# Kernel tuning notes

Hardware: AMD Instinct MI355X
Metric: run time of the kernel (lower is better)

The kernel has to match this reference:

```python
import jax, jax.numpy as jnp
import numpy as np

N = 50000        # nodes
E = 1600000      # edges (avg degree 32)
H = 128          # hidden_channels == num_filters
G = 50           # num_gaussians
L = 5            # num_interactions
CUTOFF = 4.5
VOCAB = 100
LOG2 = float(np.log(2.0))


def setup_inputs() -> dict:
    key = jax.random.key(0)
    ks = jax.random.split(key, 12)
    s = 1.0 / np.sqrt(H)
    sg = 1.0 / np.sqrt(G)
    atomic_numbers = jax.random.randint(ks[0], (N,), 0, VOCAB, dtype=jnp.int32)
    edge_index = jax.random.randint(ks[1], (2, E), 0, N, dtype=jnp.int32)
    edge_attr = jax.random.uniform(ks[2], (E,), dtype=jnp.float32)
    emb = jax.random.normal(ks[3], (VOCAB, H), dtype=jnp.float32) * 0.1
    emb = emb.at[0].set(0.0)  # padding_idx=0
    Wi = jax.random.normal(ks[4], (L, H, H), dtype=jnp.float32) * s
    bi = jnp.zeros((L, H), dtype=jnp.float32)
    Wn = jax.random.normal(ks[5], (L, G, H), dtype=jnp.float32) * sg
    bn = jnp.zeros((L, H), dtype=jnp.float32)
    Wo = jax.random.normal(ks[6], (L, H, H), dtype=jnp.float32) * s
    bo = jnp.zeros((L, H), dtype=jnp.float32)
    Wl = jax.random.normal(ks[7], (L, H, H), dtype=jnp.float32) * s
    bl = jnp.zeros((L, H), dtype=jnp.float32)
    return {"atomic_numbers": atomic_numbers, "edge_index": edge_index,
            "edge_attr": edge_attr, "emb": emb,
            "Wi": Wi, "bi": bi, "Wn": Wn, "bn": bn,
            "Wo": Wo, "bo": bo, "Wl": Wl, "bl": bl}


def _gaussian_smearing(dist):
    offsets = jnp.linspace(0.0, CUTOFF, G, dtype=jnp.float32)
    coeff = -0.5 / (offsets[1] - offsets[0]) ** 2
    return jnp.exp(coeff * (dist[:, None] - offsets[None, :]) ** 2)  # [E, G]


def reference(atomic_numbers, edge_index, edge_attr, emb,
              Wi, bi, Wn, bn, Wo, bo, Wl, bl):
    src, dst = edge_index[0], edge_index[1]
    x = emb[atomic_numbers]                      # [N, H]
    gauss = _gaussian_smearing(edge_attr)        # [E, G]
    C = 0.5 * (jnp.cos(edge_attr * jnp.pi / CUTOFF) + 1.0)  # cosine cutoff [E]
    for l in range(L):
        W = (gauss @ Wn[l] + bn[l]) * C[:, None]   # edge filters [E, H]
        h = x @ Wi[l] + bi[l]                       # [N, H]
        msg = h[src] * W                            # gather + filter [E, H]
        agg = jax.ops.segment_sum(msg, dst, num_segments=N)  # scatter-add [N, H]
        h = agg @ Wo[l] + bo[l]
        h = jax.nn.softplus(h) - LOG2               # shifted softplus
        h = h @ Wl[l] + bl[l]
        x = x + h                                   # residual
    return x
```

## Files before the change

kernel.cpp:

```cpp
#include <hip/hip_runtime.h>
#include <hip/hip_bf16.h>

#define HDIM 128
#define NG 50
#define NL 5
#define TBN 4096
#define CAP 96
#define CAPB 9000
#define CHUNK 8192

static constexpr float CUTOFF_F = 4.5f;
static constexpr float PI_F = 3.14159265358979323846f;
static constexpr float LN2_F = 0.6931471805599453f;

typedef __attribute__((ext_vector_type(8))) short bf16x8;
typedef __attribute__((ext_vector_type(4))) float f32x4;

__device__ __forceinline__ unsigned f2bfbits(float f) {
    unsigned b = __float_as_uint(f);
    return (b + 0x7FFFu + ((b >> 16) & 1u)) >> 16;
}
__device__ __forceinline__ float bflo(unsigned u) { return __uint_as_float(u << 16); }
__device__ __forceinline__ float bfhi(unsigned u) { return __uint_as_float(u & 0xFFFF0000u); }

__device__ __forceinline__ float softplus_shifted(float v) {
    return fmaxf(v, 0.0f) + __logf(1.0f + __expf(-fabsf(v))) - LN2_F;
}

__device__ __forceinline__ bf16x8 ldB(const unsigned short* __restrict__ W,
                                      int nn, int kc, int l4) {
    return *reinterpret_cast<const bf16x8*>(W + nn * HDIM + kc * 32 + l4 * 8);
}

__global__ __launch_bounds__(256) void embed_kernel(
    const int* __restrict__ an, const float* __restrict__ emb,
    float* __restrict__ x, int n)
{
    int idx = blockIdx.x * 256 + threadIdx.x;
    int total = n * (HDIM / 4);
    if (idx >= total) return;
    int i = idx >> 5;
    int j = idx & 31;
    int a = an[i];
    reinterpret_cast<float4*>(x)[(size_t)i * 32 + j] =
        reinterpret_cast<const float4*>(emb)[(size_t)a * 32 + j];
}

__global__ __launch_bounds__(256) void prep_weights(
    const float* __restrict__ Wi, const float* __restrict__ Wo,
    const float* __restrict__ Wl, unsigned short* __restrict__ Wt)
{
    int b = blockIdx.x;
    int l = b / 3, m = b % 3;
    const float* src = (m == 0 ? Wi : (m == 1 ? Wo : Wl)) + (size_t)l * HDIM * HDIM;
    unsigned short* dst = Wt + (size_t)b * HDIM * HDIM;
    for (int idx = threadIdx.x; idx < HDIM * HDIM; idx += 256) {
        int k = idx >> 7, n = idx & 127;
        dst[n * HDIM + k] = (unsigned short)f2bfbits(src[k * HDIM + n]);
    }
}

__global__ __launch_bounds__(128) void build_tables_all(
    const float* __restrict__ Wn, const float* __restrict__ bn,
    unsigned short* __restrict__ T)
{
    __shared__ float gs[NG];
    int p = blockIdx.x;
    int l = blockIdx.y;
    int j = threadIdx.x;
    const float* Wnl = Wn + (size_t)l * NG * HDIM;
    float d = (float)p * (1.0f / (float)TBN);
    if (j < NG) {
        const float delta = CUTOFF_F / (float)(NG - 1);
        const float coeff = -0.5f / (delta * delta);
        float t = d - (float)j * delta;
        gs[j] = expf(coeff * t * t);
    }
    __syncthreads();
    float acc = bn[(size_t)l * HDIM + j];
    #pragma unroll 10
    for (int g = 0; g < NG; ++g) acc = fmaf(gs[g], Wnl[g * HDIM + j], acc);
    acc *= 0.5f * (cosf(d * (PI_F / CUTOFF_F)) + 1.0f);
    T[((size_t)l * (TBN + 1) + p) * HDIM + j] = (unsigned short)f2bfbits(acc);
}

__global__ __launch_bounds__(512) void bucket_pass(
    const int* __restrict__ src, const int* __restrict__ dstp,
    const float* __restrict__ attr, int* __restrict__ gbase,
    uint2* __restrict__ buf, int E, int nbuck)
{
    __shared__ int hist[256], cur[256], base_l[256];
    const int tid = threadIdx.x;
    if (tid < 256) { hist[tid] = 0; cur[tid] = 0; }
    __syncthreads();
    const int e0 = blockIdx.x * CHUNK;
    const int e1 = min(e0 + CHUNK, E);
    for (int e = e0 + tid; e < e1; e += 512)
        atomicAdd(&hist[dstp[e] >> 8], 1);
    __syncthreads();
    if (tid < nbuck)
        base_l[tid] = hist[tid] ? atomicAdd(&gbase[tid], hist[tid]) : 0;
    __syncthreads();
    for (int e = e0 + tid; e < e1; e += 512) {
        int d = dstp[e];
        int b = d >> 8;
        int rank = atomicAdd(&cur[b], 1);
        int pos = base_l[b] + rank;
        unsigned ii = (unsigned)(int)fminf(attr[e] * (float)TBN + 0.5f, (float)TBN);
        if (pos < CAPB)
            buf[(size_t)b * CAPB + pos] = make_uint2((ii << 16) | (unsigned)src[e], (unsigned)d);
    }
}

__global__ __launch_bounds__(512) void bin_pass(
    const int* __restrict__ gtot, const uint2* __restrict__ buf,
    unsigned* __restrict__ sp, int* __restrict__ cnt, int N)
{
    __shared__ int cl[256];
    const int b = blockIdx.x;
    const int tid = threadIdx.x;
    if (tid < 256) cl[tid] = 0;
    __syncthreads();
    int total = gtot[b];
    if (total > CAPB) total = CAPB;
    const uint2* rb = buf + (size_t)b * CAPB;
    for (int i = tid; i < total; i += 512) {
        uint2 r = rb[i];
        int node = (int)r.y;
        int slot = atomicAdd(&cl[node & 255], 1);
        if (slot < CAP) sp[(size_t)node * CAP + slot] = r.x;
    }
    __syncthreads();
    if (tid < 256) {
        int node = b * 256 + tid;
        if (node < N) cnt[node] = min(cl[tid], CAP);
    }
}

__global__ __launch_bounds__(256) void mfma_gemm0(
    const float* __restrict__ A, const unsigned short* __restrict__ Wt,
    const float* __restrict__ bias, unsigned short* __restrict__ outp, int M)
{
    __shared__ unsigned short Ls[64 * HDIM];
    const int tid = threadIdx.x;
    const int row0 = blockIdx.x * 64;

    #pragma unroll
    for (int it = 0; it < 8; ++it) {
        int idx = it * 256 + tid;
        int r = idx >> 5;
        int k2 = (idx & 31) * 8;
        int row = row0 + r;
        float4 v = make_float4(0.f, 0.f, 0.f, 0.f);
        if (row < M) v = reinterpret_cast<const float4*>(A)[(size_t)row * 32 + (idx & 31)];
        uint2 u;
        u.x = f2bfbits(v.x) | (f2bfbits(v.y) << 16);
        u.y = f2bfbits(v.z) | (f2bfbits(v.w) << 16);
        *reinterpret_cast<uint2*>(reinterpret_cast<char*>(Ls) +
            r * 256 + (k2 ^ ((r & 7) << 4))) = u;
    }
    __syncthreads();

    const int wid = tid >> 6, lane = tid & 63;
    const int wr = wid >> 1, wc = wid & 1;
    const int l15 = lane & 15, l4 = lane >> 4;

    f32x4 acc[2][4] = {};
    bf16x8 afrag[2][4];
    #pragma unroll
    for (int m = 0; m < 2; ++m)
        #pragma unroll
        for (int kc = 0; kc < 4; ++kc) {
            int r = wr * 32 + m * 16 + l15;
            int k2 = (kc * 32 + l4 * 8) * 2;
            afrag[m][kc] = *reinterpret_cast<const bf16x8*>(
                reinterpret_cast<const char*>(Ls) + r * 256 + (k2 ^ ((r & 7) << 4)));
        }
    __syncthreads();
    #pragma unroll
    for (int n = 0; n < 4; ++n)
        #pragma unroll
        for (int kc = 0; kc < 4; ++kc) {
            bf16x8 bfrag = ldB(Wt, wc * 64 + n * 16 + l15, kc, l4);
            #pragma unroll
            for (int m = 0; m < 2; ++m)
                acc[m][n] = __builtin_amdgcn_mfma_f32_16x16x32_bf16(
                    afrag[m][kc], bfrag, acc[m][n], 0, 0, 0);
        }
    #pragma unroll
    for (int n = 0; n < 4; ++n) {
        int col = wc * 64 + n * 16 + l15;
        float bv = bias[col];
        #pragma unroll
        for (int m = 0; m < 2; ++m)
            #pragma unroll
            for (int r = 0; r < 4; ++r) {
                int rl = wr * 32 + m * 16 + l4 * 4 + r;
                Ls[rl * HDIM + col] = (unsigned short)f2bfbits(acc[m][n][r] + bv);
            }
    }
    __syncthreads();
    #pragma unroll
    for (int it = 0; it < 4; ++it) {
        int e = it * 256 + tid;
        int row = row0 + (e >> 4);
        if (row < M)
            reinterpret_cast<uint4*>(outp)[(size_t)row0 * 16 + e] =
                reinterpret_cast<const uint4*>(Ls)[e];
    }
}

template<int LAST>
__global__ __launch_bounds__(512) void gemm_fused(
    const unsigned short* __restrict__ aggb, const unsigned short* __restrict__ Wot,
    const float* __restrict__ bo, const unsigned short* __restrict__ Wlt,
    const float* __restrict__ bl, float* __restrict__ x,
    const unsigned short* __restrict__ Wit, const float* __restrict__ bi_,
    unsigned short* __restrict__ hb, int M)
{
    __shared__ unsigned short Ls[64 * HDIM];
    const int tid = threadIdx.x;
    const int row0 = blockIdx.x * 64;
    const int wid = tid >> 6, lane = tid & 63;
    const int wr = wid >> 1, wc = wid & 1;
    const int l15 = lane & 15, l4 = lane >> 4;

    const unsigned short* ag =
        aggb + (size_t)(row0 + wr * 16 + l15) * HDIM + l4 * 8;
    f32x4 acc1[4] = {};
    bf16x8 af[4];
    #pragma unroll
    for (int kc = 0; kc < 4; ++kc)
        af[kc] = *reinterpret_cast<const bf16x8*>(ag + kc * 32);
    #pragma unroll
    for (int n = 0; n < 4; ++n)
        #pragma unroll
        for (int kc = 0; kc < 4; ++kc) {
            bf16x8 bfrag = ldB(Wot, wc * 64 + n * 16 + l15, kc, l4);
            acc1[n] = __builtin_amdgcn_mfma_f32_16x16x32_bf16(af[kc], bfrag, acc1[n], 0, 0, 0);
        }

    #pragma unroll
    for (int n = 0; n < 4; ++n) {
        int col = wc * 64 + n * 16 + l15;
        float bv = bo[col];
        #pragma unroll
        for (int r = 0; r < 4; ++r) {
            int rl = wr * 16 + l4 * 4 + r;
            float v = softplus_shifted(acc1[n][r] + bv);
            *reinterpret_cast<unsigned short*>(reinterpret_cast<char*>(Ls) +
                rl * 256 + ((2 * col) ^ ((rl & 7) << 4))) = (unsigned short)f2bfbits(v);
        }
    }
    __syncthreads();

    {
        int r = wr * 16 + l15;
        #pragma unroll
        for (int kc = 0; kc < 4; ++kc) {
            int k2 = (kc * 32 + l4 * 8) * 2;
            af[kc] = *reinterpret_cast<const bf16x8*>(
                reinterpret_cast<const char*>(Ls) + r * 256 + (k2 ^ ((r & 7) << 4)));
        }
    }
    __syncthreads();
    f32x4 acc2[4] = {};
    #pragma unroll
    for (int n = 0; n < 4; ++n)
        #pragma unroll
        for (int kc = 0; kc < 4; ++kc) {
            bf16x8 bfrag = ldB(Wlt, wc * 64 + n * 16 + l15, kc, l4);
            acc2[n] = __builtin_amdgcn_mfma_f32_16x16x32_bf16(af[kc], bfrag, acc2[n], 0, 0, 0);
        }

    #pragma unroll
    for (int n = 0; n < 4; ++n) {
        int col = wc * 64 + n * 16 + l15;
        float bv = bl[col];
        #pragma unroll
        for (int r = 0; r < 4; ++r) {
            int rl = wr * 16 + l4 * 4 + r;
            int row = row0 + rl;
            float v = acc2[n][r] + bv;
            if (row < M) {
                float* o = x + (size_t)row * HDIM + col;
                v += *o;
                *o = v;
            }
            if (!LAST)
                *reinterpret_cast<unsigned short*>(reinterpret_cast<char*>(Ls) +
                    rl * 256 + ((2 * col) ^ ((rl & 7) << 4))) = (unsigned short)f2bfbits(v);
        }
    }
    if (LAST) return;
    __syncthreads();

    {
        int r = wr * 16 + l15;
        #pragma unroll
        for (int kc = 0; kc < 4; ++kc) {
            int k2 = (kc * 32 + l4 * 8) * 2;
            af[kc] = *reinterpret_cast<const bf16x8*>(
                reinterpret_cast<const char*>(Ls) + r * 256 + (k2 ^ ((r & 7) << 4)));
        }
    }
    __syncthreads();
    f32x4 acc3[4] = {};
    #pragma unroll
    for (int n = 0; n < 4; ++n)
        #pragma unroll
        for (int kc = 0; kc < 4; ++kc) {
            bf16x8 bfrag = ldB(Wit, wc * 64 + n * 16 + l15, kc, l4);
            acc3[n] = __builtin_amdgcn_mfma_f32_16x16x32_bf16(af[kc], bfrag, acc3[n], 0, 0, 0);
        }
    #pragma unroll
    for (int n = 0; n < 4; ++n) {
        int col = wc * 64 + n * 16 + l15;
        float bv = bi_[col];
        #pragma unroll
        for (int r = 0; r < 4; ++r) {
            int rl = wr * 16 + l4 * 4 + r;
            Ls[rl * HDIM + col] = (unsigned short)f2bfbits(acc3[n][r] + bv);
        }
    }
    __syncthreads();
    #pragma unroll
    for (int it = 0; it < 2; ++it) {
        int e = it * 512 + tid;
        int row = row0 + (e >> 4);
        if (row < M)
            reinterpret_cast<uint4*>(hb)[(size_t)row0 * 16 + e] =
                reinterpret_cast<const uint4*>(Ls)[e];
    }
}

__global__ __launch_bounds__(256) void agg_kernel(
    const int* __restrict__ cnt, const unsigned* __restrict__ sp,
    const unsigned short* __restrict__ T,
    const unsigned* __restrict__ hb,
    unsigned* __restrict__ aggb, int n)
{
    __shared__ float2 part[2][64];
    const int tid = threadIdx.x;
    const int lane = tid & 63;
    const int wv = tid >> 6;
    const int pair = wv >> 1, half = wv & 1;
    const int node = blockIdx.x * 2 + pair;

    int deg = (node < n) ? cnt[node] : 0;
    const unsigned* recs = sp + (size_t)node * CAP;
    int d2 = deg >> 1;
    int i  = half ? d2 : 0;
    int i1 = half ? deg : d2;
    float ax = 0.0f, ay = 0.0f;

    for (; i + 8 <= i1; i += 8) {
        unsigned rec[8], tv[8], hv[8];
        #pragma unroll
        for (int k = 0; k < 8; ++k) rec[k] = recs[i + k];
        #pragma unroll
        for (int k = 0; k < 8; ++k) {
            tv[k] = reinterpret_cast<const unsigned*>(T + (size_t)(rec[k] >> 16) * HDIM)[lane];
            hv[k] = hb[(size_t)(rec[k] & 0xFFFFu) * 64 + lane];
        }
        #pragma unroll
        for (int k = 0; k < 8; ++k) {
            ax = fmaf(bflo(hv[k]), bflo(tv[k]), ax);
            ay = fmaf(bfhi(hv[k]), bfhi(tv[k]), ay);
        }
    }
    if (i + 4 <= i1) {
        unsigned rec[4], tv[4], hv[4];
        #pragma unroll
        for (int k = 0; k < 4; ++k) rec[k] = recs[i + k];
        #pragma unroll
        for (int k = 0; k < 4; ++k) {
            tv[k] = reinterpret_cast<const unsigned*>(T + (size_t)(rec[k] >> 16) * HDIM)[lane];
            hv[k] = hb[(size_t)(rec[k] & 0xFFFFu) * 64 + lane];
        }
        #pragma unroll
        for (int k = 0; k < 4; ++k) {
            ax = fmaf(bflo(hv[k]), bflo(tv[k]), ax);
            ay = fmaf(bfhi(hv[k]), bfhi(tv[k]), ay);
        }
        i += 4;
    }
    for (; i < i1; ++i) {
        unsigned rec = recs[i];
        unsigned tvv = reinterpret_cast<const unsigned*>(T + (size_t)(rec >> 16) * HDIM)[lane];
        unsigned hvv = hb[(size_t)(rec & 0xFFFFu) * 64 + lane];
        ax = fmaf(bflo(hvv), bflo(tvv), ax);
        ay = fmaf(bfhi(hvv), bfhi(tvv), ay);
    }

    if (half) part[pair][lane] = make_float2(ax, ay);
    __syncthreads();
    if (!half && node < n) {
        float2 p = part[pair][lane];
        ax += p.x; ay += p.y;
        aggb[(size_t)node * 64 + lane] = f2bfbits(ax) | (f2bfbits(ay) << 16);
    }
}

extern "C" void kernel_launch(void* const* d_in, const int* in_sizes, int n_in,
                              void* d_out, int out_size, void* d_ws, size_t ws_size,
                              hipStream_t stream)
{
    const int*   an   = (const int*)d_in[0];
    const int*   ei   = (const int*)d_in[1];
    const float* attr = (const float*)d_in[2];
    const float* emb  = (const float*)d_in[3];
    const float* Wi   = (const float*)d_in[4];
    const float* bi   = (const float*)d_in[5];
    const float* Wn   = (const float*)d_in[6];
    const float* bn   = (const float*)d_in[7];
    const float* Wo   = (const float*)d_in[8];
    const float* bo   = (const float*)d_in[9];
    const float* Wl   = (const float*)d_in[10];
    const float* bl   = (const float*)d_in[11];

    const int N = in_sizes[0];
    const int E = in_sizes[2];
    const int* srcp = ei;
    const int* dstp = ei + E;
    const int nbuck = (N + 255) >> 8;

    float* x = (float*)d_out;

    char* w = (char*)d_ws;
    unsigned*       aggb = (unsigned*)w;      w += (size_t)N * HDIM * 2;
    unsigned*       hb   = (unsigned*)w;      w += (size_t)N * HDIM * 2;
    unsigned short* T    = (unsigned short*)w; w += (size_t)NL * (TBN + 1) * HDIM * 2;
    unsigned short* Wt   = (unsigned short*)w; w += (size_t)NL * 3 * HDIM * HDIM * 2;
    int*            cnt  = (int*)w;           w += (size_t)N * 4;
    int*            gbase= (int*)w;           w += 256 * 4;
    unsigned*       sp   = (unsigned*)w;      w += (size_t)N * CAP * 4;
    uint2*          buf  = (uint2*)aggb;

    prep_weights<<<NL * 3, 256, 0, stream>>>(Wi, Wo, Wl, Wt);
    embed_kernel<<<(N * 32 + 255) / 256, 256, 0, stream>>>(an, emb, x, N);
    build_tables_all<<<dim3(TBN + 1, NL), 128, 0, stream>>>(Wn, bn, T);

    hipMemsetAsync(gbase, 0, 256 * sizeof(int), stream);
    bucket_pass<<<(E + CHUNK - 1) / CHUNK, 512, 0, stream>>>(
        srcp, dstp, attr, gbase, buf, E, nbuck);
    bin_pass<<<nbuck, 512, 0, stream>>>(gbase, buf, sp, cnt, N);

    const int gemm_grid = (N + 63) / 64;
    const int agg_grid  = (N + 1) / 2;

    mfma_gemm0<<<gemm_grid, 256, 0, stream>>>(x, Wt, bi, (unsigned short*)hb, N);

    for (int l = 0; l < NL; ++l) {
        agg_kernel<<<agg_grid, 256, 0, stream>>>(
            cnt, sp, T + (size_t)l * (TBN + 1) * HDIM, hb, aggb, N);
        if (l < NL - 1) {
            gemm_fused<0><<<gemm_grid, 512, 0, stream>>>(
                (unsigned short*)aggb, Wt + (size_t)(l * 3 + 1) * HDIM * HDIM, bo + (size_t)l * HDIM,
                Wt + (size_t)(l * 3 + 2) * HDIM * HDIM, bl + (size_t)l * HDIM, x,
                Wt + (size_t)((l + 1) * 3 + 0) * HDIM * HDIM, bi + (size_t)(l + 1) * HDIM,
                (unsigned short*)hb, N);
        } else {
            gemm_fused<1><<<gemm_grid, 512, 0, stream>>>(
                (unsigned short*)aggb, Wt + (size_t)(l * 3 + 1) * HDIM * HDIM, bo + (size_t)l * HDIM,
                Wt + (size_t)(l * 3 + 2) * HDIM * HDIM, bl + (size_t)l * HDIM, x,
                Wt, bi, (unsigned short*)hb, N);
        }
    }
}
```

Baseline: 835.5 us.

## Restructure aggregation to one wave per node with 16-byte gathers

Measured after the change: 757.7 us. 9.3% less time.

```diff
diff --git a/kernel.cpp b/kernel.cpp
--- a/kernel.cpp
+++ b/kernel.cpp
@@ -94,15 +94,22 @@
     if (tid < 256) { hist[tid] = 0; cur[tid] = 0; }
     __syncthreads();
     const int e0 = blockIdx.x * CHUNK;
-    const int e1 = min(e0 + CHUNK, E);
-    for (int e = e0 + tid; e < e1; e += 512)
-        atomicAdd(&hist[dstp[e] >> 8], 1);
+    int myd[CHUNK / 512];
+    #pragma unroll
+    for (int k = 0; k < CHUNK / 512; ++k) {
+        int e = e0 + k * 512 + tid;
+        myd[k] = (e < E) ? dstp[e] : -1;
+        if (myd[k] >= 0) atomicAdd(&hist[myd[k] >> 8], 1);
+    }
     __syncthreads();
     if (tid < nbuck)
         base_l[tid] = hist[tid] ? atomicAdd(&gbase[tid], hist[tid]) : 0;
     __syncthreads();
-    for (int e = e0 + tid; e < e1; e += 512) {
-        int d = dstp[e];
+    #pragma unroll
+    for (int k = 0; k < CHUNK / 512; ++k) {
+        int d = myd[k];
+        if (d < 0) continue;
+        int e = e0 + k * 512 + tid;
         int b = d >> 8;
         int rank = atomicAdd(&cur[b], 1);
         int pos = base_l[b] + rank;
@@ -334,71 +341,69 @@
     }
 }
 
+#define ACC8(hv, tv) \
+    a0 = fmaf(bflo(hv.x), bflo(tv.x), a0); a1 = fmaf(bfhi(hv.x), bfhi(tv.x), a1); \
+    a2 = fmaf(bflo(hv.y), bflo(tv.y), a2); a3 = fmaf(bfhi(hv.y), bfhi(tv.y), a3); \
+    a4 = fmaf(bflo(hv.z), bflo(tv.z), a4); a5 = fmaf(bfhi(hv.z), bfhi(tv.z), a5); \
+    a6 = fmaf(bflo(hv.w), bflo(tv.w), a6); a7 = fmaf(bfhi(hv.w), bfhi(tv.w), a7);
+
 __global__ __launch_bounds__(256) void agg_kernel(
     const int* __restrict__ cnt, const unsigned* __restrict__ sp,
     const unsigned short* __restrict__ T,
     const unsigned* __restrict__ hb,
     unsigned* __restrict__ aggb, int n)
 {
-    __shared__ float2 part[2][64];
     const int tid = threadIdx.x;
     const int lane = tid & 63;
-    const int wv = tid >> 6;
-    const int pair = wv >> 1, half = wv & 1;
-    const int node = blockIdx.x * 2 + pair;
-
-    int deg = (node < n) ? cnt[node] : 0;
+    const int g = lane >> 4;
+    const int c16 = lane & 15;
+    const int node = (blockIdx.x * 256 + tid) >> 6;
+    if (node >= n) return;
+
+    const int deg = cnt[node];
     const unsigned* recs = sp + (size_t)node * CAP;
-    int d2 = deg >> 1;
-    int i  = half ? d2 : 0;
-    int i1 = half ? deg : d2;
-    float ax = 0.0f, ay = 0.0f;
-
-    for (; i + 8 <= i1; i += 8) {
-        unsigned rec[8], tv[8], hv[8];
-        #pragma unroll
-        for (int k = 0; k < 8; ++k) rec[k] = recs[i + k];
-        #pragma unroll
-        for (int k = 0; k < 8; ++k) {
-            tv[k] = reinterpret_cast<const unsigned*>(T + (size_t)(rec[k] >> 16) * HDIM)[lane];
-            hv[k] = hb[(size_t)(rec[k] & 0xFFFFu) * 64 + lane];
-        }
-        #pragma unroll
-        for (int k = 0; k < 8; ++k) {
-            ax = fmaf(bflo(hv[k]), bflo(tv[k]), ax);
-            ay = fmaf(bfhi(hv[k]), bfhi(tv[k]), ay);
-        }
-    }
-    if (i + 4 <= i1) {
-        unsigned rec[4], tv[4], hv[4];
-        #pragma unroll
-        for (int k = 0; k < 4; ++k) rec[k] = recs[i + k];
-        #pragma unroll
-        for (int k = 0; k < 4; ++k) {
-            tv[k] = reinterpret_cast<const unsigned*>(T + (size_t)(rec[k] >> 16) * HDIM)[lane];
-            hv[k] = hb[(size_t)(rec[k] & 0xFFFFu) * 64 + lane];
-        }
-        #pragma unroll
-        for (int k = 0; k < 4; ++k) {
-            ax = fmaf(bflo(hv[k]), bflo(tv[k]), ax);
-            ay = fmaf(bfhi(hv[k]), bfhi(tv[k]), ay);
-        }
-        i += 4;
-    }
-    for (; i < i1; ++i) {
-        unsigned rec = recs[i];
-        unsigned tvv = reinterpret_cast<const unsigned*>(T + (size_t)(rec >> 16) * HDIM)[lane];
-        unsigned hvv = hb[(size_t)(rec & 0xFFFFu) * 64 + lane];
-        ax = fmaf(bflo(hvv), bflo(tvv), ax);
-        ay = fmaf(bfhi(hvv), bfhi(tvv), ay);
-    }
-
-    if (half) part[pair][lane] = make_float2(ax, ay);
-    __syncthreads();
-    if (!half && node < n) {
-        float2 p = part[pair][lane];
-        ax += p.x; ay += p.y;
-        aggb[(size_t)node * 64 + lane] = f2bfbits(ax) | (f2bfbits(ay) << 16);
+    const uint4* T4 = reinterpret_cast<const uint4*>(T);
+    const uint4* h4 = reinterpret_cast<const uint4*>(hb);
+
+    float a0 = 0.f, a1 = 0.f, a2 = 0.f, a3 = 0.f;
+    float a4 = 0.f, a5 = 0.f, a6 = 0.f, a7 = 0.f;
+
+    int i = 0;
+    for (; i + 8 <= deg; i += 8) {
+        unsigned ra = recs[i + g];
+        unsigned rb = recs[i + 4 + g];
+        uint4 ta = T4[(size_t)(ra >> 16) * 16 + c16];
+        uint4 ha = h4[(size_t)(ra & 0xFFFFu) * 16 + c16];
+        uint4 tb = T4[(size_t)(rb >> 16) * 16 + c16];
+        uint4 hbv = h4[(size_t)(rb & 0xFFFFu) * 16 + c16];
+        ACC8(ha, ta)
+        ACC8(hbv, tb)
+    }
+    for (int base = i; base < deg; base += 4) {
+        int e = base + g;
+        unsigned r = (e < deg) ? recs[e] : 0u;
+        uint4 tv = T4[(size_t)(r >> 16) * 16 + c16];
+        uint4 hv = make_uint4(0u, 0u, 0u, 0u);
+        if (e < deg) hv = h4[(size_t)(r & 0xFFFFu) * 16 + c16];
+        ACC8(hv, tv)
+    }
+
+    a0 += __shfl_xor(a0, 16); a1 += __shfl_xor(a1, 16);
+    a2 += __shfl_xor(a2, 16); a3 += __shfl_xor(a3, 16);
+    a4 += __shfl_xor(a4, 16); a5 += __shfl_xor(a5, 16);
+    a6 += __shfl_xor(a6, 16); a7 += __shfl_xor(a7, 16);
+    a0 += __shfl_xor(a0, 32); a1 += __shfl_xor(a1, 32);
+    a2 += __shfl_xor(a2, 32); a3 += __shfl_xor(a3, 32);
+    a4 += __shfl_xor(a4, 32); a5 += __shfl_xor(a5, 32);
+    a6 += __shfl_xor(a6, 32); a7 += __shfl_xor(a7, 32);
+
+    if (g == 0) {
+        uint4 o;
+        o.x = f2bfbits(a0) | (f2bfbits(a1) << 16);
+        o.y = f2bfbits(a2) | (f2bfbits(a3) << 16);
+        o.z = f2bfbits(a4) | (f2bfbits(a5) << 16);
+        o.w = f2bfbits(a6) | (f2bfbits(a7) << 16);
+        reinterpret_cast<uint4*>(aggb)[(size_t)node * 16 + c16] = o;
     }
 }
 
@@ -447,7 +452,7 @@
     bin_pass<<<nbuck, 512, 0, stream>>>(gbase, buf, sp, cnt, N);
 
     const int gemm_grid = (N + 63) / 64;
-    const int agg_grid  = (N + 1) / 2;
+    const int agg_grid  = (N + 3) / 4;
 
     mfma_gemm0<<<gemm_grid, 256, 0, stream>>>(x, Wt, bi, (unsigned short*)hb, N);
 
```
